# Optimization experiments

Hardware: AMD Instinct MI355X
Metric: run time of the kernel (lower is better)

## Reference

```python
import jax, jax.numpy as jnp
import numpy as np

KH, KW = 3, 3  # window_size[1], window_size[2]
FILTERS = 64
CHANNELS = 32
K = KH * KW * CHANNELS


def _extract_patches_valid(x, kh, kw):
    # TF tf.image.extract_patches ordering: (row_offset, col_offset, channel)
    B, H, W, C = x.shape
    Ho, Wo = H - kh + 1, W - kw + 1
    cols = [x[:, i:i + Ho, j:j + Wo, :] for i in range(kh) for j in range(kw)]
    return jnp.concatenate(cols, axis=-1)  # (B, Ho, Wo, kh*kw*C)


def setup_inputs() -> dict:
    key = jax.random.key(0)
    kx, kw = jax.random.split(key)
    x = jax.random.normal(kx, (8, 32, 32, CHANNELS), dtype=jnp.float32)
    # learned weight per __init__: shape (1, 1, 1, K, filters), random_normal init
    w = jax.random.normal(kw, (1, 1, 1, K, FILTERS), dtype=jnp.float32) * 0.05
    return {"x": x, "w": w}


def reference(x, w):
    # patches: (B, Ho, Wo, K)
    patches = _extract_patches_valid(x, KH, KW)
    # broadcast-add against weights: (B, Ho, Wo, K, filters)
    s = patches[..., None] + w[0, 0, 0]  # w[0,0,0]: (K, filters)
    # tropical conv: max over patch axis minus min over patch axis
    return jnp.max(s, axis=3) - jnp.min(s, axis=3)  # (B, Ho, Wo, filters)
```

## Files before the change

kernel.cpp:

```cpp
#include <hip/hip_runtime.h>


#define C_IN 32
#define NF 64
#define H_OUT 30
#define W_OUT 30
#define W_IN 32

static __device__ __forceinline__ float max3f(float a, float b, float c) {
    return fmaxf(fmaxf(a, b), c);
}
static __device__ __forceinline__ float min3f(float a, float b, float c) {
    return fminf(fminf(a, b), c);
}

__global__ __launch_bounds__(512) void tropconv_kernel(
    const float* __restrict__ x,
    const float* __restrict__ w,
    float* __restrict__ out) {
    const int bx = blockIdx.x;
    const int q = bx & 3;
    const int bho = bx >> 2;
    const int b = bho / H_OUT;
    const int ho = bho - b * H_OUT;
    const int tid = threadIdx.x;
    const int lane = tid & 63;
    const int wave = tid >> 6;

    const int col0 = q * 8;
    const int npx = (q == 3) ? 6 : 8;
    const int ncols = (q == 3) ? 8 : 10;

    __shared__ __align__(16) float xs[3 * 10 * C_IN];
    __shared__ float pmx[8][8][NF];
    __shared__ float pmn[8][8][NF];

    {
        const int nf4_row = ncols * (C_IN / 4);
        const int total_f4 = 3 * nf4_row;
        if (tid < total_f4) {
            const int r = tid / nf4_row;
            const int cc = tid - r * nf4_row;
            const float4* __restrict__ src = (const float4*)(
                x + ((size_t)((b * 32 + ho + r) * W_IN + col0)) * C_IN);
            ((float4*)xs)[r * 80 + cc] = src[cc];
        }
    }

    const float* __restrict__ wbase = w + (size_t)(wave * 4) * NF + lane;

    float wc[4];
    #pragma unroll
    for (int cc = 0; cc < 4; ++cc) wc[cc] = wbase[cc * NF];

    __syncthreads();

    float mx[8], mn[8];
    #pragma unroll
    for (int t = 0; t < 8; ++t) { mx[t] = -INFINITY; mn[t] = INFINITY; }

    #pragma unroll
    for (int ij = 0; ij < 9; ++ij) {
        float wn[4];
        if (ij < 8) {
            #pragma unroll
            for (int cc = 0; cc < 4; ++cc)
                wn[cc] = wbase[((ij + 1) * C_IN + cc) * NF];
        }

        const int i = ij / 3;
        const int j = ij - i * 3;
        const float* __restrict__ xrow = xs + (i * 10 + j) * C_IN + wave * 4;

        #pragma unroll
        for (int px = 0; px < 8; ++px) {
            float4 p = *(const float4*)(xrow + px * C_IN);
            float s0 = p.x + wc[0];
            float s1 = p.y + wc[1];
            float s2 = p.z + wc[2];
            float s3 = p.w + wc[3];
            mx[px] = max3f(max3f(s0, s1, s2), s3, mx[px]);
            mn[px] = min3f(min3f(s0, s1, s2), s3, mn[px]);
        }

        #pragma unroll
        for (int cc = 0; cc < 4; ++cc) wc[cc] = wn[cc];
    }

    #pragma unroll
    for (int px = 0; px < 8; ++px) {
        pmx[wave][px][lane] = mx[px];
        pmn[wave][px][lane] = mn[px];
    }
    __syncthreads();

    const int nout = npx * NF;
    if (tid < nout) {
        const int px = tid >> 6;
        const int f = tid & 63;
        float a = fmaxf(fmaxf(fmaxf(pmx[0][px][f], pmx[1][px][f]),
                              fmaxf(pmx[2][px][f], pmx[3][px][f])),
                        fmaxf(fmaxf(pmx[4][px][f], pmx[5][px][f]),
                              fmaxf(pmx[6][px][f], pmx[7][px][f])));
        float m = fminf(fminf(fminf(pmn[0][px][f], pmn[1][px][f]),
                              fminf(pmn[2][px][f], pmn[3][px][f])),
                        fminf(fminf(pmn[4][px][f], pmn[5][px][f]),
                              fminf(pmn[6][px][f], pmn[7][px][f])));
        out[((size_t)bho * W_OUT + (col0 + px)) * NF + f] = a - m;
    }
}

extern "C" void kernel_launch(void* const* d_in, const int* in_sizes, int n_in,
                              void* d_out, int out_size, void* d_ws, size_t ws_size,
                              hipStream_t stream) {
    const float* x = (const float*)d_in[0];
    const float* w = (const float*)d_in[1];
    float* out = (float*)d_out;

    dim3 grid(8 * H_OUT * 4);
    dim3 block(512);
    tropconv_kernel<<<grid, block, 0, stream>>>(x, w, out);
}
```

Baseline: 63.29 us.

## Drop LDS staging of input tile; load wave-uniform x rows directly from global

Removes the shared-memory staging of the 3x10 input window and its barrier. Each wave now reads its four channels as float4 loads straight from global memory, with a wave-uniform address made scalar via readfirstlane, and the column index is clamped for the partial last tile. The loop is reorganised by kernel row so weights for a whole row are loaded together and overlapping columns are reused across adjacent output pixels. This removes one synchronisation and the LDS round trip, but relies on cache for the repeated global reads and raises register use.

```diff
diff --git a/kernel.cpp b/kernel.cpp
--- a/kernel.cpp
+++ b/kernel.cpp
@@ -25,72 +25,65 @@
     const int ho = bho - b * H_OUT;
     const int tid = threadIdx.x;
     const int lane = tid & 63;
-    const int wave = tid >> 6;
+    const int wave = __builtin_amdgcn_readfirstlane(tid >> 6);
 
     const int col0 = q * 8;
     const int npx = (q == 3) ? 6 : 8;
-    const int ncols = (q == 3) ? 8 : 10;
+    const int cmax = (q == 3) ? 7 : 9;
 
-    __shared__ __align__(16) float xs[3 * 10 * C_IN];
     __shared__ float pmx[8][8][NF];
     __shared__ float pmn[8][8][NF];
-
-    {
-        const int nf4_row = ncols * (C_IN / 4);
-        const int total_f4 = 3 * nf4_row;
-        if (tid < total_f4) {
-            const int r = tid / nf4_row;
-            const int cc = tid - r * nf4_row;
-            const float4* __restrict__ src = (const float4*)(
-                x + ((size_t)((b * 32 + ho + r) * W_IN + col0)) * C_IN);
-            ((float4*)xs)[r * 80 + cc] = src[cc];
-        }
-    }
-
-    const float* __restrict__ wbase = w + (size_t)(wave * 4) * NF + lane;
-
-    float wc[4];
-    #pragma unroll
-    for (int cc = 0; cc < 4; ++cc) wc[cc] = wbase[cc * NF];
-
-    __syncthreads();
 
     float mx[8], mn[8];
     #pragma unroll
     for (int t = 0; t < 8; ++t) { mx[t] = -INFINITY; mn[t] = INFINITY; }
 
+    const float* __restrict__ wbase = w + (size_t)(wave * 4) * NF + lane;
+
     #pragma unroll
-    for (int ij = 0; ij < 9; ++ij) {
-        float wn[4];
-        if (ij < 8) {
+    for (int i = 0; i < 3; ++i) {
+        float wr[12];
+        #pragma unroll
+        for (int j = 0; j < 3; ++j)
             #pragma unroll
-            for (int cc = 0; cc < 4; ++cc)
-                wn[cc] = wbase[((ij + 1) * C_IN + cc) * NF];
-        }
+            for (int c = 0; c < 4; ++c)
+                wr[j * 4 + c] = wbase[((i * 3 + j) * C_IN + c) * NF];
 
-        const int i = ij / 3;
-        const int j = ij - i * 3;
-        const float* __restrict__ xrow = xs + (i * 10 + j) * C_IN + wave * 4;
+        const float4* __restrict__ row4 = (const float4*)(
+            x + ((size_t)((b * 32 + ho + i) * W_IN + col0)) * C_IN) + wave;
 
         #pragma unroll
-        for (int px = 0; px < 8; ++px) {
-            float4 p = *(const float4*)(xrow + px * C_IN);
-            float s0 = p.x + wc[0];
-            float s1 = p.y + wc[1];
-            float s2 = p.z + wc[2];
-            float s3 = p.w + wc[3];
-            mx[px] = max3f(max3f(s0, s1, s2), s3, mx[px]);
-            mn[px] = min3f(min3f(s0, s1, s2), s3, mn[px]);
+        for (int half = 0; half < 2; ++half) {
+            float4 p[6];
+            #pragma unroll
+            for (int t = 0; t < 6; ++t) {
+                int col = half * 4 + t;
+                if (col > cmax) col = cmax;
+                p[t] = row4[col * 8];
+            }
+            #pragma unroll
+            for (int px = 0; px < 4; ++px) {
+                const int g = half * 4 + px;
+                float s0  = p[px].x     + wr[0],  s1  = p[px].y     + wr[1];
+                float s2  = p[px].z     + wr[2],  s3  = p[px].w     + wr[3];
+                float s4  = p[px + 1].x + wr[4],  s5  = p[px + 1].y + wr[5];
+                float s6  = p[px + 1].z + wr[6],  s7  = p[px + 1].w + wr[7];
+                float s8  = p[px + 2].x + wr[8],  s9  = p[px + 2].y + wr[9];
+                float s10 = p[px + 2].z + wr[10], s11 = p[px + 2].w + wr[11];
+                mx[g] = max3f(max3f(max3f(s0, s1, s2), max3f(s3, s4, s5),
+                                    max3f(s6, s7, s8)),
+                              max3f(s9, s10, s11), mx[g]);
+                mn[g] = min3f(min3f(min3f(s0, s1, s2), min3f(s3, s4, s5),
+                                    min3f(s6, s7, s8)),
+                              min3f(s9, s10, s11), mn[g]);
+            }
         }
-
-        #pragma unroll
-        for (int cc = 0; cc < 4; ++cc) wc[cc] = wn[cc];
     }
 
     #pragma unroll
-    for (int px = 0; px < 8; ++px) {
-        pmx[wave][px][lane] = mx[px];
-        pmn[wave][px][lane] = mn[px];
+    for (int t = 0; t < 8; ++t) {
+        pmx[wave][t][lane] = mx[t];
+        pmn[wave][t][lane] = mn[t];
     }
     __syncthreads();
 
```

Result: no change. 63.90 us (+1.0%).
